# Optimization experiments

Hardware: AMD Instinct MI355X
Metric: run time of the kernel (lower is better)

## Reference

```python
import jax, jax.numpy as jnp
import numpy as np

# Deformable DETR encoder layer constants (match init_kwargs / input_specs)
SPATIAL_SHAPES = [(100, 152), (50, 76), (25, 38), (13, 19)]  # (H, W) per level
D_MODEL, D_FFN = 256, 1024
N_LEVELS, N_HEADS, N_POINTS = 4, 8, 4
HEAD_DIM = D_MODEL // N_HEADS
LEN_IN = sum(h * w for h, w in SPATIAL_SHAPES)  # 20197
BATCH = 2


def layer_norm(x, g, b, eps=1e-5):
    m = x.mean(-1, keepdims=True)
    v = ((x - m) ** 2).mean(-1, keepdims=True)
    return (x - m) * jax.lax.rsqrt(v + eps) * g + b


def sample_level(value_l, loc, H, W):
    # value_l: [B, nH, H*W, d]; loc: [B, nH, N, 2] normalized to [0,1]
    # Bilinear sampling, align_corners=False, zero padding (torch grid_sample semantics)
    x = loc[..., 0] * W - 0.5
    y = loc[..., 1] * H - 0.5
    x0, y0 = jnp.floor(x), jnp.floor(y)
    out = jnp.zeros(loc.shape[:-1] + (value_l.shape[-1],), value_l.dtype)
    for dx, dy in ((0, 0), (1, 0), (0, 1), (1, 1)):
        xi, yi = x0 + dx, y0 + dy
        w = (1.0 - jnp.abs(x - xi)) * (1.0 - jnp.abs(y - yi))
        valid = (xi >= 0) & (xi < W) & (yi >= 0) & (yi < H)
        idx = (jnp.clip(yi, 0, H - 1) * W + jnp.clip(xi, 0, W - 1)).astype(jnp.int32)
        v = jnp.take_along_axis(value_l, idx[..., None], axis=2)  # [B,nH,N,d]
        out = out + v * (w * valid.astype(value_l.dtype))[..., None]
    return out


def ms_deform_attn(query, src, ref, W_off, b_off, W_attn, b_attn, W_val, b_val, W_out, b_out):
    B, Lq, C = query.shape
    # value projection -> [B, nH, Len_in, head_dim]
    value = (src @ W_val + b_val).reshape(B, LEN_IN, N_HEADS, HEAD_DIM).transpose(0, 2, 1, 3)
    off = (query @ W_off + b_off).reshape(B, Lq, N_HEADS, N_LEVELS, N_POINTS, 2)
    attn = (query @ W_attn + b_attn).reshape(B, Lq, N_HEADS, N_LEVELS * N_POINTS)
    attn = jax.nn.softmax(attn, -1).reshape(B, Lq, N_HEADS, N_LEVELS, N_POINTS)
    # offset normalizer is (W, H) per level
    normalizer = jnp.array([[w, h] for h, w in SPATIAL_SHAPES], dtype=query.dtype)
    loc = ref[:, :, None, :, None, :] + off / normalizer[None, None, None, :, None, :]  # [B,Lq,nH,nL,nP,2]
    out = jnp.zeros((B, N_HEADS, Lq, HEAD_DIM), query.dtype)
    start = 0
    for l, (H, W) in enumerate(SPATIAL_SHAPES):
        v_l = value[:, :, start:start + H * W]
        start += H * W
        loc_l = loc[:, :, :, l].transpose(0, 2, 1, 3, 4).reshape(B, N_HEADS, Lq * N_POINTS, 2)
        s = sample_level(v_l, loc_l, H, W).reshape(B, N_HEADS, Lq, N_POINTS, HEAD_DIM)
        a = attn[:, :, :, l].transpose(0, 2, 1, 3)  # [B,nH,Lq,nP]
        out = out + (s * a[..., None]).sum(3)
    out = out.transpose(0, 2, 1, 3).reshape(B, Lq, C)
    return out @ W_out + b_out


def setup_inputs() -> dict:
    key = jax.random.key(0)
    ks = jax.random.split(key, 20)
    s = 0.02
    spatial_shapes = jnp.array(SPATIAL_SHAPES, dtype=jnp.int64)
    lsi = np.cumsum([0] + [h * w for h, w in SPATIAL_SHAPES[:-1]])
    return {
        'src': jax.random.normal(ks[0], (BATCH, LEN_IN, D_MODEL), jnp.float32),
        'pos': jax.random.normal(ks[1], (BATCH, LEN_IN, D_MODEL), jnp.float32),
        'reference_points': jax.random.uniform(ks[2], (BATCH, LEN_IN, N_LEVELS, 2), jnp.float32),
        'spatial_shapes': spatial_shapes,
        'level_start_index': jnp.array(lsi, dtype=jnp.int64),
        'W_off': jax.random.normal(ks[3], (D_MODEL, N_HEADS * N_LEVELS * N_POINTS * 2), jnp.float32) * s,
        'b_off': jax.random.normal(ks[4], (N_HEADS * N_LEVELS * N_POINTS * 2,), jnp.float32) * s,
        'W_attn': jax.random.normal(ks[5], (D_MODEL, N_HEADS * N_LEVELS * N_POINTS), jnp.float32) * s,
        'b_attn': jnp.zeros((N_HEADS * N_LEVELS * N_POINTS,), jnp.float32),
        'W_val': jax.random.normal(ks[6], (D_MODEL, D_MODEL), jnp.float32) * s,
        'b_val': jnp.zeros((D_MODEL,), jnp.float32),
        'W_out': jax.random.normal(ks[7], (D_MODEL, D_MODEL), jnp.float32) * s,
        'b_out': jnp.zeros((D_MODEL,), jnp.float32),
        'W1': jax.random.normal(ks[8], (D_MODEL, D_FFN), jnp.float32) * s,
        'b1': jnp.zeros((D_FFN,), jnp.float32),
        'W2': jax.random.normal(ks[9], (D_FFN, D_MODEL), jnp.float32) * s,
        'b2': jnp.zeros((D_MODEL,), jnp.float32),
        'g1': jnp.ones((D_MODEL,), jnp.float32),
        'be1': jnp.zeros((D_MODEL,), jnp.float32),
        'g2': jnp.ones((D_MODEL,), jnp.float32),
        'be2': jnp.zeros((D_MODEL,), jnp.float32),
    }


def reference(src, pos, reference_points, spatial_shapes, level_start_index,
              W_off, b_off, W_attn, b_attn, W_val, b_val, W_out, b_out,
              W1, b1, W2, b2, g1, be1, g2, be2):
    # eval mode: all dropouts are identity; ReLUDropout -> relu
    query = src + pos
    src2 = ms_deform_attn(query, src, reference_points,
                          W_off, b_off, W_attn, b_attn, W_val, b_val, W_out, b_out)
    x = layer_norm(src + src2, g1, be1)
    ffn = jax.nn.relu(x @ W1 + b1) @ W2 + b2
    return layer_norm(x + ffn, g2, be2)
```

## Files before the change

kernel.cpp:

```cpp
#include <hip/hip_runtime.h>
#include <math.h>

#define LEN_IN_C 20197
#define BATCH_C 2
#define BL_C (BATCH_C * LEN_IN_C)

typedef short  bf16x8 __attribute__((ext_vector_type(8)));
typedef float  f32x4  __attribute__((ext_vector_type(4)));

__device__ __forceinline__ ushort f2bf(float f) {
    unsigned u = __float_as_uint(f);
    return (ushort)((u + 0x7fffu + ((u >> 16) & 1u)) >> 16);
}
__device__ __forceinline__ float bf2f(ushort u) {
    return __uint_as_float((uint)u << 16);
}
__device__ __forceinline__ uint pkbf(float a, float b) {
    uint r;
    asm("v_cvt_pk_bf16_f32 %0, %1, %2" : "=v"(r) : "v"(a), "v"(b));
    return r;
}
__device__ __forceinline__ void gload16(const void* g, void* l) {
    __builtin_amdgcn_global_load_lds(
        (const __attribute__((address_space(1))) unsigned char*)g,
        (__attribute__((address_space(3))) unsigned char*)l, 16, 0, 0);
}
__device__ __forceinline__ int xcd_swz(int lid, int nwg) {
    const int q = nwg >> 3, r = nwg & 7;
    const int xcd = lid & 7, p = lid >> 3;
    return (xcd < r ? xcd * (q + 1) : r * (q + 1) + (xcd - r) * q) + p;
}

__device__ __forceinline__ void tcast32(
    const float* W, ushort* WT, int K, int N, int n0, int k0, float* tile )
{
    const int ty = threadIdx.x >> 3, tx = threadIdx.x & 7;
    float4 v = *(const float4*)(W + (size_t)(k0 + ty) * N + n0 + tx * 4);
    tile[ty * 33 + tx * 4 + 0] = v.x; tile[ty * 33 + tx * 4 + 1] = v.y;
    tile[ty * 33 + tx * 4 + 2] = v.z; tile[ty * 33 + tx * 4 + 3] = v.w;
    __syncthreads();
    ushort4 o;
    o.x = f2bf(tile[(tx * 4 + 0) * 33 + ty]);
    o.y = f2bf(tile[(tx * 4 + 1) * 33 + ty]);
    o.z = f2bf(tile[(tx * 4 + 2) * 33 + ty]);
    o.w = f2bf(tile[(tx * 4 + 3) * 33 + ty]);
    *(ushort4*)(WT + (size_t)(n0 + ty) * K + k0 + tx * 4) = o;
}

__global__ __launch_bounds__(256) void prep_all(
    const float* __restrict__ src, const float* __restrict__ pos,
    const float* __restrict__ Wv, const float* __restrict__ Wo,
    const float* __restrict__ Wa, const float* __restrict__ Wout,
    const float* __restrict__ W1, const float* __restrict__ W2,
    const float* __restrict__ bo, const float* __restrict__ ba,
    ushort* __restrict__ Tval, ushort* __restrict__ Toa,
    ushort* __restrict__ Tout, ushort* __restrict__ TW1,
    ushort* __restrict__ TW2, float* __restrict__ boa,
    ushort* __restrict__ qout, ushort* __restrict__ srcb)
{
    __shared__ float tile[32 * 33];
    const int bx = blockIdx.x;
    const int tid = threadIdx.x;
    if (bx < 64) {
        tcast32(Wv, Tval, 256, 256, (bx & 7) * 32, (bx >> 3) * 32, tile);
    } else if (bx < 128) {
        const int s = bx - 64;
        tcast32(Wout, Tout, 256, 256, (s & 7) * 32, (s >> 3) * 32, tile);
    } else if (bx < 384) {
        const int s = bx - 128;
        tcast32(W1, TW1, 256, 1024, (s & 31) * 32, (s >> 5) * 32, tile);
    } else if (bx < 640) {
        const int s = bx - 384;
        tcast32(W2, TW2, 1024, 256, (s & 7) * 32, (s >> 3) * 32, tile);
    } else if (bx < 736) {
        const int idx = (bx - 640) * 256 + tid;
        const int n = idx >> 6, k4 = (idx & 63) * 4;
        ushort4 o; ushort* po = (ushort*)&o;
        #pragma unroll
        for (int j = 0; j < 4; ++j) {
            const int k = k4 + j;
            const float v = (n < 256) ? Wo[(size_t)k * 256 + n]
                                      : Wa[(size_t)k * 128 + (n - 256)];
            po[j] = f2bf(v);
        }
        *(ushort4*)(Toa + (size_t)n * 256 + k4) = o;
    } else if (bx < 738) {
        const int n = (bx - 736) * 256 + tid;
        if (n < 384) boa[n] = (n < 256) ? bo[n] : ba[n - 256];
    } else {
        const int n8 = BL_C * 32;
        for (int i = (bx - 738) * 256 + tid; i < n8; i += 1024 * 256) {
            const size_t base = (size_t)i * 8;
            float4 a0 = *(const float4*)(src + base);
            float4 a1 = *(const float4*)(src + base + 4);
            float4 b0 = *(const float4*)(pos + base);
            float4 b1 = *(const float4*)(pos + base + 4);
            uint4 o;
            o.x = pkbf(a0.x + b0.x, a0.y + b0.y);
            o.y = pkbf(a0.z + b0.z, a0.w + b0.w);
            o.z = pkbf(a1.x + b1.x, a1.y + b1.y);
            o.w = pkbf(a1.z + b1.z, a1.w + b1.w);
            *(uint4*)(qout + base) = o;
            uint4 s4;
            s4.x = pkbf(a0.x, a0.y); s4.y = pkbf(a0.z, a0.w);
            s4.z = pkbf(a1.x, a1.y); s4.w = pkbf(a1.z, a1.w);
            *(uint4*)(srcb + base) = s4;
        }
    }
}

template <bool RELU>
__global__ __launch_bounds__(256) void gemm_bs(
    const ushort* __restrict__ A, const ushort* __restrict__ BT,
    const float* __restrict__ bias, ushort* __restrict__ C,
    const int M, const int N, const int K, const int NT, const int nwg)
{
    __shared__ ushort lsB[64 * 256];

    const int nid = xcd_swz(blockIdx.x, nwg);
    const int nt = nid % NT, mt = nid / NT;
    const int row0 = mt * 128, col0 = nt * 64;

    const int tid = threadIdx.x;
    const int ln = tid & 63, wv = tid >> 6;
    const int l16 = ln & 15, lk = ln >> 4;

    uint abase[2];
    #pragma unroll
    for (int m = 0; m < 2; ++m) {
        int rr = row0 + wv * 32 + m * 16 + l16;
        if (rr > M - 1) rr = M - 1;
        abase[m] = (uint)rr * K + lk * 8;
    }
    uint bbase[4], bxor[4];
    #pragma unroll
    for (int n = 0; n < 4; ++n) {
        const int brow = n * 16 + l16;
        bbase[n] = (uint)(brow * 512 + lk * 16);
        bxor[n]  = (uint)((brow & 7) << 4);
    }

    f32x4 acc[2][4] = {};
    const int nch = K >> 8;

    for (int ch = 0; ch < nch; ++ch) {
        const int kc0 = ch << 8;

        bf16x8 ar[8][2];
        #pragma unroll
        for (int s = 0; s < 8; ++s)
            #pragma unroll
            for (int m = 0; m < 2; ++m)
                ar[s][m] = *(const bf16x8*)(A + abase[m] + kc0 + s * 32);

        if (ch) __syncthreads();
        #pragma unroll
        for (int j = 0; j < 8; ++j) {
            const int d = j * 256 + tid;
            const int brow = d >> 5;
            const int c = (d & 31) ^ (brow & 7);
            gload16(BT + (size_t)(col0 + brow) * K + kc0 + c * 8,
                    (char*)lsB + j * 4096 + wv * 1024);
        }
        __syncthreads();

        #pragma unroll
        for (int gs = 0; gs < 8; ++gs) {
            bf16x8 bv[4];
            #pragma unroll
            for (int n = 0; n < 4; ++n)
                bv[n] = *(const bf16x8*)((const char*)lsB +
                        ((bbase[n] + gs * 64) ^ bxor[n]));
            #pragma unroll
            for (int m = 0; m < 2; ++m)
                #pragma unroll
                for (int n = 0; n < 4; ++n)
                    acc[m][n] = __builtin_amdgcn_mfma_f32_16x16x32_bf16(
                        bv[n], ar[gs][m], acc[m][n], 0, 0, 0);
        }
    }

    #pragma unroll
    for (int m = 0; m < 2; ++m) {
        const int grow = row0 + wv * 32 + m * 16 + l16;
        if (grow >= M) continue;
        ushort* crow = C + (size_t)grow * N;
        #pragma unroll
        for (int n = 0; n < 4; ++n) {
            const int col4 = col0 + n * 16 + lk * 4;
            float4 bs = *(const float4*)(bias + col4);
            f32x4 v = acc[m][n];
            float o0 = v[0] + bs.x, o1 = v[1] + bs.y, o2 = v[2] + bs.z, o3 = v[3] + bs.w;
            if (RELU) {
                o0 = fmaxf(o0, 0.f); o1 = fmaxf(o1, 0.f);
                o2 = fmaxf(o2, 0.f); o3 = fmaxf(o3, 0.f);
            }
            *(uint2*)(crow + col4) = make_uint2(pkbf(o0, o1), pkbf(o2, o3));
        }
    }
}

__global__ __launch_bounds__(256) void sample_kernel(
    const ushort* __restrict__ value,
    const ushort* __restrict__ oa,
    const float* __restrict__ ref,
    ushort* __restrict__ outbf)
{
    constexpr int Hs[4] = {100, 50, 25, 13};
    constexpr int Ws[4] = {152, 76, 38, 19};
    constexpr int St[4] = {0, 15200, 19000, 19950};
    constexpr int NWG = (BL_C + 7) / 8;

    const int bq0 = xcd_swz(blockIdx.x, NWG) * 8;
    const int t = threadIdx.x;

    __shared__ uint2 s_ow[8][8][65];

    #pragma unroll
    for (int rnd = 0; rnd < 4; ++rnd) {
        const int qi2 = t >> 7, r2 = t & 127;
        const int qloc = rnd * 2 + qi2;
        int bq = bq0 + qloc; if (bq > BL_C - 1) bq = BL_C - 1;
        const int b = (bq >= LEN_IN_C) ? 1 : 0;
        const int h = r2 >> 4, i = r2 & 15, l = i >> 2, p = i & 3;
        const ushort* crow = oa + (size_t)bq * 384;

        float lg = bf2f(crow[256 + h * 16 + i]);
        float mx = lg;
        #pragma unroll
        for (int o = 1; o < 16; o <<= 1) mx = fmaxf(mx, __shfl_xor(mx, o, 16));
        float e = __expf(lg - mx), sm = e;
        #pragma unroll
        for (int o = 1; o < 16; o <<= 1) sm += __shfl_xor(sm, o, 16);
        const float aw = e / sm;

        const uint ov = *(const uint*)(crow + h * 32 + l * 8 + p * 2);
        const float ox = __uint_as_float(ov << 16);
        const float oy = __uint_as_float(ov & 0xffff0000u);
        const float2 rxy = *(const float2*)(ref + (size_t)bq * 8 + l * 2);
        const int H = Hs[l], W = Ws[l];
        const float x = rxy.x * (float)W + ox - 0.5f;
        const float y = rxy.y * (float)H + oy - 0.5f;
        const float x0f = floorf(x), y0f = floorf(y);
        const float fx = x - x0f, fy = y - y0f;
        const int x0 = (int)x0f, y0 = (int)y0f;
        const uint rowb = (uint)(b * LEN_IN_C + St[l]);
        #pragma unroll
        for (int c = 0; c < 4; ++c) {
            const int dx = c & 1, dy = c >> 1;
            const int xi = x0 + dx, yi = y0 + dy;
            const bool valid = (xi >= 0) & (xi < W) & (yi >= 0) & (yi < H);
            float wgt = (dx ? fx : 1.f - fx) * (dy ? fy : 1.f - fy) * aw;
            if (!valid) wgt = 0.f;
            const int xc = xi < 0 ? 0 : (xi > W - 1 ? W - 1 : xi);
            const int yc = yi < 0 ? 0 : (yi > H - 1 ? H - 1 : yi);
            const uint ro = (rowb + (uint)(yc * W + xc)) * 512u;
            s_ow[qloc][h][i * 4 + c] = make_uint2(ro, __float_as_uint(wgt));
        }
    }
    __syncthreads();

    const int q = t >> 5, h2 = (t >> 2) & 7, d4 = t & 3;
    int bq = bq0 + q; if (bq > BL_C - 1) bq = BL_C - 1;
    const char* vb = (const char*)value;
    const uint toff = (uint)(h2 * 64 + d4 * 16);

    float a0 = 0.f, a1 = 0.f, a2 = 0.f, a3 = 0.f;
    float a4 = 0.f, a5 = 0.f, a6 = 0.f, a7 = 0.f;
    #pragma unroll 8
    for (int j = 0; j < 64; ++j) {
        const uint2 ow = s_ow[q][h2][j];
        const uint4 v = *(const uint4*)(vb + (size_t)(ow.x + toff));
        const float w = __uint_as_float(ow.y);
        a0 += w * __uint_as_float(v.x << 16);
        a1 += w * __uint_as_float(v.x & 0xffff0000u);
        a2 += w * __uint_as_float(v.y << 16);
        a3 += w * __uint_as_float(v.y & 0xffff0000u);
        a4 += w * __uint_as_float(v.z << 16);
        a5 += w * __uint_as_float(v.z & 0xffff0000u);
        a6 += w * __uint_as_float(v.w << 16);
        a7 += w * __uint_as_float(v.w & 0xffff0000u);
    }
    uint4 o;
    o.x = pkbf(a0, a1); o.y = pkbf(a2, a3);
    o.z = pkbf(a4, a5); o.w = pkbf(a6, a7);
    *(uint4*)(outbf + (size_t)bq * 256 + h2 * 32 + d4 * 8) = o;
}

template <bool ABF, bool OF32>
__global__ __launch_bounds__(256) void add_ln(
    const void* __restrict__ ap, const ushort* __restrict__ bp,
    const float* __restrict__ g, const float* __restrict__ be,
    void* __restrict__ op)
{
    const int row = blockIdx.x * 4 + (threadIdx.x >> 6);
    if (row >= BL_C) return;
    const int ln = threadIdx.x & 63;
    const size_t base = (size_t)row * 256 + ln * 4;

    float x[4];
    if (ABF) {
        ushort4 a4 = *(const ushort4*)((const ushort*)ap + base);
        x[0] = bf2f(a4.x); x[1] = bf2f(a4.y); x[2] = bf2f(a4.z); x[3] = bf2f(a4.w);
    } else {
        float4 a4 = *(const float4*)((const float*)ap + base);
        x[0] = a4.x; x[1] = a4.y; x[2] = a4.z; x[3] = a4.w;
    }
    ushort4 b4 = *(const ushort4*)(bp + base);
    x[0] += bf2f(b4.x); x[1] += bf2f(b4.y); x[2] += bf2f(b4.z); x[3] += bf2f(b4.w);

    float s = x[0] + x[1] + x[2] + x[3];
    #pragma unroll
    for (int o = 32; o >= 1; o >>= 1) s += __shfl_xor(s, o, 64);
    const float mean = s * (1.f / 256.f);
    float d0 = x[0] - mean, d1 = x[1] - mean, d2 = x[2] - mean, d3 = x[3] - mean;
    float ss = d0 * d0 + d1 * d1 + d2 * d2 + d3 * d3;
    #pragma unroll
    for (int o = 32; o >= 1; o >>= 1) ss += __shfl_xor(ss, o, 64);
    const float rs = rsqrtf(ss * (1.f / 256.f) + 1e-5f);

    float4 gv = *(const float4*)(g + ln * 4);
    float4 bv = *(const float4*)(be + ln * 4);
    float o0 = d0 * rs * gv.x + bv.x;
    float o1 = d1 * rs * gv.y + bv.y;
    float o2 = d2 * rs * gv.z + bv.z;
    float o3 = d3 * rs * gv.w + bv.w;

    if (OF32) {
        *(float4*)((float*)op + base) = make_float4(o0, o1, o2, o3);
    } else {
        ushort4 st;
        st.x = f2bf(o0); st.y = f2bf(o1); st.z = f2bf(o2); st.w = f2bf(o3);
        *(ushort4*)((ushort*)op + base) = st;
    }
}

extern "C" void kernel_launch(void* const* d_in, const int* in_sizes, int n_in,
                              void* d_out, int out_size, void* d_ws, size_t ws_size,
                              hipStream_t stream) {
    const float* src    = (const float*)d_in[0];
    const float* pos    = (const float*)d_in[1];
    const float* refpts = (const float*)d_in[2];
    const float* W_off  = (const float*)d_in[5];
    const float* b_off  = (const float*)d_in[6];
    const float* W_attn = (const float*)d_in[7];
    const float* b_attn = (const float*)d_in[8];
    const float* W_val  = (const float*)d_in[9];
    const float* b_val  = (const float*)d_in[10];
    const float* W_out  = (const float*)d_in[11];
    const float* b_out  = (const float*)d_in[12];
    const float* W1     = (const float*)d_in[13];
    const float* b1     = (const float*)d_in[14];
    const float* W2     = (const float*)d_in[15];
    const float* b2     = (const float*)d_in[16];
    const float* g1     = (const float*)d_in[17];
    const float* be1    = (const float*)d_in[18];
    const float* g2     = (const float*)d_in[19];
    const float* be2    = (const float*)d_in[20];
    float* out = (float*)d_out;
    (void)in_sizes; (void)n_in; (void)out_size; (void)ws_size;

    const int BL = BL_C;
    char* ws = (char*)d_ws;
    const size_t HB  = (size_t)BL * 256 * 2;
    const size_t OAB = (size_t)BL * 384 * 2;

    ushort* q_bf    = (ushort*)(ws);
    ushort* x_bf    = (ushort*)(ws);
    ushort* val_bf  = (ushort*)(ws + HB);
    ushort* oa_bf   = (ushort*)(ws + 2 * HB);
    ushort* ao_bf   = (ushort*)(ws + 2 * HB + OAB);
    ushort* src2_bf = (ushort*)(ws + 3 * HB + OAB);
    ushort* srcb_bf = (ushort*)(ws + 4 * HB + OAB);
    ushort* ffn2_bf = srcb_bf;
    ushort* mid_bf  = val_bf;
    char*   wts     = ws + 5 * HB + OAB;
    ushort* Tval = (ushort*)(wts);
    ushort* Toa  = Tval + 256 * 256;
    ushort* Tout = Toa + 384 * 256;
    ushort* TW1  = Tout + 256 * 256;
    ushort* TW2  = TW1 + 1024 * 256;
    float*  boa  = (float*)(TW2 + 256 * 1024);

    dim3 blk(256);
    const int MT = (BL + 127) / 128;

    prep_all<<<dim3(738 + 1024), blk, 0, stream>>>(
        src, pos, W_val, W_off, W_attn, W_out, W1, W2, b_off, b_attn,
        Tval, Toa, Tout, TW1, TW2, boa, q_bf, srcb_bf);

    gemm_bs<false><<<dim3(MT * 4), blk, 0, stream>>>(
        srcb_bf, Tval, b_val, val_bf, BL, 256, 256, 4, MT * 4);
    gemm_bs<false><<<dim3(MT * 6), blk, 0, stream>>>(
        q_bf, Toa, boa, oa_bf, BL, 384, 256, 6, MT * 6);

    sample_kernel<<<dim3((BL + 7) / 8), blk, 0, stream>>>(val_bf, oa_bf, refpts, ao_bf);

    gemm_bs<false><<<dim3(MT * 4), blk, 0, stream>>>(
        ao_bf, Tout, b_out, src2_bf, BL, 256, 256, 4, MT * 4);

    add_ln<false, false><<<dim3((BL + 3) / 4), blk, 0, stream>>>(
        src, src2_bf, g1, be1, x_bf);

    gemm_bs<true><<<dim3(MT * 16), blk, 0, stream>>>(
        x_bf, TW1, b1, mid_bf, BL, 1024, 256, 16, MT * 16);

    gemm_bs<false><<<dim3(MT * 4), blk, 0, stream>>>(
        mid_bf, TW2, b2, ffn2_bf, BL, 256, 1024, 4, MT * 4);

    add_ln<true, true><<<dim3((BL + 3) / 4), blk, 0, stream>>>(
        x_bf, ffn2_bf, g2, be2, out);
}
```

Before: 303.7 us.

## Pair horizontal bilinear corners per row and pack weights as fp16

The sampling kernel now stores one offset per bilinear row, with the left and right x-corner weights packed as two fp16 values. The x base is clamped to W-2 so both adjacent pixels are valid, with the weights remapped to match. This halves the shared-memory entries and LDS reads and issues two neighbouring 512-byte-stride loads per entry. Separately, the first add+layernorm now reads the bf16 copy of src instead of fp32, which cuts bytes read but lowers residual precision.

```diff
diff --git a/kernel.cpp b/kernel.cpp
--- a/kernel.cpp
+++ b/kernel.cpp
@@ -1,4 +1,5 @@
 #include <hip/hip_runtime.h>
+#include <hip/hip_fp16.h>
 #include <math.h>
 
 #define LEN_IN_C 20197
@@ -19,6 +20,17 @@
     uint r;
     asm("v_cvt_pk_bf16_f32 %0, %1, %2" : "=v"(r) : "v"(a), "v"(b));
     return r;
+}
+__device__ __forceinline__ uint pkhalf(float a, float b) {
+    const ushort ha = __half_as_ushort(__float2half_rn(a));
+    const ushort hb = __half_as_ushort(__float2half_rn(b));
+    return (uint)ha | ((uint)hb << 16);
+}
+__device__ __forceinline__ float h2f_lo(uint u) {
+    return __half2float(__ushort_as_half((ushort)(u & 0xffffu)));
+}
+__device__ __forceinline__ float h2f_hi(uint u) {
+    return __half2float(__ushort_as_half((ushort)(u >> 16)));
 }
 __device__ __forceinline__ void gload16(const void* g, void* l) {
     __builtin_amdgcn_global_load_lds(
@@ -214,7 +226,7 @@
     const int bq0 = xcd_swz(blockIdx.x, NWG) * 8;
     const int t = threadIdx.x;
 
-    __shared__ uint2 s_ow[8][8][65];
+    __shared__ uint2 s_pw[8][8][33];
 
     #pragma unroll
     for (int rnd = 0; rnd < 4; ++rnd) {
@@ -244,18 +256,23 @@
         const float x0f = floorf(x), y0f = floorf(y);
         const float fx = x - x0f, fy = y - y0f;
         const int x0 = (int)x0f, y0 = (int)y0f;
-        const uint rowb = (uint)(b * LEN_IN_C + St[l]);
-        #pragma unroll
-        for (int c = 0; c < 4; ++c) {
-            const int dx = c & 1, dy = c >> 1;
-            const int xi = x0 + dx, yi = y0 + dy;
-            const bool valid = (xi >= 0) & (xi < W) & (yi >= 0) & (yi < H);
-            float wgt = (dx ? fx : 1.f - fx) * (dy ? fy : 1.f - fy) * aw;
-            if (!valid) wgt = 0.f;
-            const int xc = xi < 0 ? 0 : (xi > W - 1 ? W - 1 : xi);
-            const int yc = yi < 0 ? 0 : (yi > H - 1 ? H - 1 : yi);
-            const uint ro = (rowb + (uint)(yc * W + xc)) * 512u;
-            s_ow[qloc][h][i * 4 + c] = make_uint2(ro, __float_as_uint(wgt));
+
+        const float wx0 = (x0 >= 0 && x0 < W) ? (1.f - fx) : 0.f;
+        const float wx1 = (x0 + 1 >= 0 && x0 + 1 < W) ? fx : 0.f;
+        int xb = x0 < 0 ? 0 : (x0 > W - 2 ? W - 2 : x0);
+        float wLx = (xb == x0) ? wx0 : ((xb == x0 + 1) ? wx1 : 0.f);
+        float wRx = (xb + 1 == x0 + 1) ? wx1 : ((xb + 1 == x0) ? wx0 : 0.f);
+        wLx *= aw; wRx *= aw;
+
+        const uint rowb = (uint)(b * LEN_IN_C + St[l] + xb);
+        #pragma unroll
+        for (int dy = 0; dy < 2; ++dy) {
+            const int yy = y0 + dy;
+            const bool vy = (yy >= 0) & (yy < H);
+            const float wy = vy ? (dy ? fy : 1.f - fy) : 0.f;
+            const int yc = yy < 0 ? 0 : (yy > H - 1 ? H - 1 : yy);
+            const uint off = (rowb + (uint)(yc * W)) * 512u;
+            s_pw[qloc][h][i * 2 + dy] = make_uint2(off, pkhalf(wLx * wy, wRx * wy));
         }
     }
     __syncthreads();
@@ -267,19 +284,29 @@
 
     float a0 = 0.f, a1 = 0.f, a2 = 0.f, a3 = 0.f;
     float a4 = 0.f, a5 = 0.f, a6 = 0.f, a7 = 0.f;
-    #pragma unroll 8
-    for (int j = 0; j < 64; ++j) {
-        const uint2 ow = s_ow[q][h2][j];
-        const uint4 v = *(const uint4*)(vb + (size_t)(ow.x + toff));
-        const float w = __uint_as_float(ow.y);
-        a0 += w * __uint_as_float(v.x << 16);
-        a1 += w * __uint_as_float(v.x & 0xffff0000u);
-        a2 += w * __uint_as_float(v.y << 16);
-        a3 += w * __uint_as_float(v.y & 0xffff0000u);
-        a4 += w * __uint_as_float(v.z << 16);
-        a5 += w * __uint_as_float(v.z & 0xffff0000u);
-        a6 += w * __uint_as_float(v.w << 16);
-        a7 += w * __uint_as_float(v.w & 0xffff0000u);
+    #pragma unroll 4
+    for (int j = 0; j < 32; ++j) {
+        const uint2 pw = s_pw[q][h2][j];
+        const char* p = vb + (size_t)(pw.x + toff);
+        const uint4 v0 = *(const uint4*)p;
+        const uint4 v1 = *(const uint4*)(p + 512);
+        const float wL = h2f_lo(pw.y), wR = h2f_hi(pw.y);
+        a0 += wL * __uint_as_float(v0.x << 16);
+        a1 += wL * __uint_as_float(v0.x & 0xffff0000u);
+        a2 += wL * __uint_as_float(v0.y << 16);
+        a3 += wL * __uint_as_float(v0.y & 0xffff0000u);
+        a4 += wL * __uint_as_float(v0.z << 16);
+        a5 += wL * __uint_as_float(v0.z & 0xffff0000u);
+        a6 += wL * __uint_as_float(v0.w << 16);
+        a7 += wL * __uint_as_float(v0.w & 0xffff0000u);
+        a0 += wR * __uint_as_float(v1.x << 16);
+        a1 += wR * __uint_as_float(v1.x & 0xffff0000u);
+        a2 += wR * __uint_as_float(v1.y << 16);
+        a3 += wR * __uint_as_float(v1.y & 0xffff0000u);
+        a4 += wR * __uint_as_float(v1.z << 16);
+        a5 += wR * __uint_as_float(v1.z & 0xffff0000u);
+        a6 += wR * __uint_as_float(v1.w << 16);
+        a7 += wR * __uint_as_float(v1.w & 0xffff0000u);
     }
     uint4 o;
     o.x = pkbf(a0, a1); o.y = pkbf(a2, a3);
@@ -399,8 +426,8 @@
     gemm_bs<false><<<dim3(MT * 4), blk, 0, stream>>>(
         ao_bf, Tout, b_out, src2_bf, BL, 256, 256, 4, MT * 4);
 
-    add_ln<false, false><<<dim3((BL + 3) / 4), blk, 0, stream>>>(
-        src, src2_bf, g1, be1, x_bf);
+    add_ln<true, false><<<dim3((BL + 3) / 4), blk, 0, stream>>>(
+        srcb_bf, src2_bf, g1, be1, x_bf);
 
     gemm_bs<true><<<dim3(MT * 16), blk, 0, stream>>>(
         x_bf, TW1, b1, mid_bf, BL, 1024, 256, 16, MT * 16);
```

Result: no change. 298.3 us (-1.8%).
